# Optimization experiments

Hardware: AMD Instinct MI355X
Metric: run time of the kernel (lower is better)

Reference implementation:

```python
import jax, jax.numpy as jnp
import numpy as np

N_NODES = 50000
N_EDGES = 800000
N_GRAPHS = 512
D_NODE = 64
D_EDGE = 32
Z_DIM = 2 * D_NODE + D_EDGE  # 160


def setup_inputs() -> dict:
    key = jax.random.key(0)
    ks = jax.random.split(key, 12)
    inp = {
        'x': jax.random.normal(ks[0], (N_NODES, D_NODE), dtype=jnp.float32),
        'edge_index': jax.random.randint(ks[1], (2, N_EDGES), 0, N_NODES, dtype=jnp.int64),
        'edge_attr': jax.random.uniform(ks[2], (N_EDGES, D_EDGE), dtype=jnp.float32),
        'batch': jnp.sort(jax.random.randint(ks[3], (N_NODES,), 0, N_GRAPHS, dtype=jnp.int64)),
        'Wf1': jax.random.normal(ks[4], (Z_DIM, D_NODE), dtype=jnp.float32) * 0.05,
        'bf1': jnp.zeros((D_NODE,), dtype=jnp.float32),
        'Ws1': jax.random.normal(ks[5], (Z_DIM, D_NODE), dtype=jnp.float32) * 0.05,
        'bs1': jnp.zeros((D_NODE,), dtype=jnp.float32),
        'Wf2': jax.random.normal(ks[6], (Z_DIM, D_NODE), dtype=jnp.float32) * 0.05,
        'bf2': jnp.zeros((D_NODE,), dtype=jnp.float32),
        'Ws2': jax.random.normal(ks[7], (Z_DIM, D_NODE), dtype=jnp.float32) * 0.05,
        'bs2': jnp.zeros((D_NODE,), dtype=jnp.float32),
        'W_out': jax.random.normal(ks[8], (D_NODE, 1), dtype=jnp.float32) * 0.05,
        'b_out': jnp.zeros((1,), dtype=jnp.float32),
    }
    return inp


def _cgconv(x, edge_index, edge_attr, Wf, bf, Ws, bs):
    # PyG CGConv: out_i = x_i + sum_{j in N(i)} sigmoid(lin_f(z_ij)) * softplus(lin_s(z_ij))
    # with z_ij = [x_i, x_j, e_ij]; source_to_target flow: j=edge_index[0], i=edge_index[1]
    src, dst = edge_index[0], edge_index[1]
    z = jnp.concatenate([x[dst], x[src], edge_attr], axis=-1)  # [E, 2d+dim]
    msg = jax.nn.sigmoid(z @ Wf + bf) * jax.nn.softplus(z @ Ws + bs)  # [E, d]
    aggr = jax.ops.segment_sum(msg, dst, num_segments=x.shape[0])
    return x + aggr


def reference(x, edge_index, edge_attr, batch, Wf1, bf1, Ws1, bs1, Wf2, bf2, Ws2, bs2, W_out, b_out):
    h = _cgconv(x, edge_index, edge_attr, Wf1, bf1, Ws1, bs1)
    h = _cgconv(h, edge_index, edge_attr, Wf2, bf2, Ws2, bs2)
    pooled = jax.ops.segment_sum(h, batch, num_segments=N_GRAPHS)  # global_add_pool [G, d]
    out = pooled @ W_out + b_out  # [G, 1]
    return out
```

## Files before the change

### kernel.cpp

```cpp
#include <hip/hip_runtime.h>
#include <math.h>

#define N_NODES 50000
#define N_EDGES 800000
#define N_GRAPHS 512
#define D 64
#define DE 32
#define NB_SCAN 196
#define NSTR 136
#define NB_SCAT 3125
#define NB_FUSED 4689
#define NB_EDGE 1563


typedef __attribute__((ext_vector_type(8))) short short8;
typedef __attribute__((ext_vector_type(4))) float floatx4;
union Frag { short8 s; unsigned u[4]; };
union U4   { uint4 v; unsigned u[4]; };

__device__ inline unsigned pk_bf16(float lo, float hi) {
    unsigned a = __float_as_uint(lo);
    unsigned b = __float_as_uint(hi);
    a = (a + 0x7FFFu + ((a >> 16) & 1u)) >> 16;
    b = (b + 0x7FFFu + ((b >> 16) & 1u)) >> 16;
    return a | (b << 16);
}
__device__ inline unsigned short bf16_1(float v) {
    unsigned a = __float_as_uint(v);
    return (unsigned short)((a + 0x7FFFu + ((a >> 16) & 1u)) >> 16);
}
__device__ inline float upk(unsigned u16) { return __uint_as_float(u16 << 16); }

__global__ __launch_bounds__(256) void setup_kernel(
    const float* __restrict__ Wf1, const float* __restrict__ Ws1,
    const float* __restrict__ Wf2, const float* __restrict__ Ws2,
    uint4* __restrict__ WpkNT, uint4* __restrict__ WpkE,
    int* __restrict__ deg, float* __restrict__ pooled)
{
    const int b = blockIdx.x;
    if (b >= 206) {
        int i = (b - 206) * 256 + threadIdx.x;
        if (i < N_GRAPHS * D) pooled[i] = 0.0f;
        return;
    }
    if (b >= 10) {
        int i = (b - 10) * 256 + threadIdx.x;
        if (i < N_NODES) deg[i] = 0;
        return;
    }
    const int layer = b / 5;
    const float* Wf = layer ? Wf2 : Wf1;
    const float* Ws = layer ? Ws2 : Ws1;
    const int i = (b % 5) * 256 + threadIdx.x;
    if (i < 1024) {
        const int p    = i >> 9;
        const int cbi  = (i >> 6) & 7;
        const int l    = i & 63;
        const int n16  = l & 15, quad = l >> 4, kc = quad * 8;
        const int col  = cbi * 16 + n16;
        const int j    = col >> 1;
        const float* Wsel = (col & 1) ? Ws : Wf;
        const int rbase = p * 64;
        U4 b0, b1;
#pragma unroll
        for (int pp = 0; pp < 4; ++pp) {
            b0.u[pp] = pk_bf16(Wsel[(rbase + kc + 2 * pp) * 64 + j],
                               Wsel[(rbase + kc + 2 * pp + 1) * 64 + j]);
            b1.u[pp] = pk_bf16(Wsel[(rbase + 32 + kc + 2 * pp) * 64 + j],
                               Wsel[(rbase + 32 + kc + 2 * pp + 1) * 64 + j]);
        }
        uint4* o = WpkNT + ((size_t)layer * 1024 + i) * 2;
        o[0] = b0.v; o[1] = b1.v;
    } else if (i < 1280) {
        const int k  = i - 1024;
        const int jb = k >> 6;
        const int l  = k & 63;
        const int n16 = l & 15, quad = l >> 4, c0 = quad * 8;
        const int j = jb * 16 + n16;
        U4 bf_, bs_;
#pragma unroll
        for (int pp = 0; pp < 4; ++pp) {
            bf_.u[pp] = pk_bf16(Wf[(128 + c0 + 2 * pp) * 64 + j],
                                Wf[(128 + c0 + 2 * pp + 1) * 64 + j]);
            bs_.u[pp] = pk_bf16(Ws[(128 + c0 + 2 * pp) * 64 + j],
                                Ws[(128 + c0 + 2 * pp + 1) * 64 + j]);
        }
        uint4* o = WpkE + ((size_t)layer * 256 + k) * 2;
        o[0] = bf_.v; o[1] = bs_.v;
    }
}

__global__ __launch_bounds__(256) void hist_kernel(
    const int* __restrict__ ei, int* __restrict__ deg, int* __restrict__ rank)
{
    int e = blockIdx.x * 256 + threadIdx.x;
    rank[e] = atomicAdd(&deg[ei[N_EDGES + e]], 1);
}

__global__ __launch_bounds__(256) void scan1(
    const int* __restrict__ deg, int* __restrict__ off, int* __restrict__ tsum)
{
    __shared__ int s[256];
    int i = blockIdx.x * 256 + threadIdx.x;
    s[threadIdx.x] = (i < N_NODES) ? deg[i] : 0;
    __syncthreads();
    if (threadIdx.x == 0) {
        int run = 0;
        for (int k = 0; k < 256; ++k) { int t = s[k]; s[k] = run; run += t; }
        tsum[blockIdx.x] = run;
    }
    __syncthreads();
    if (i < N_NODES) off[i] = s[threadIdx.x];
}

__global__ __launch_bounds__(256) void scan23(
    int* __restrict__ off, const int* __restrict__ tsum)
{
    __shared__ int pfx;
    if (threadIdx.x == 0) {
        int run = 0;
        for (int k = 0; k < (int)blockIdx.x; ++k) run += tsum[k];
        pfx = run;
    }
    __syncthreads();
    int i = blockIdx.x * 256 + threadIdx.x;
    if (i < N_NODES) off[i] += pfx;
    if (i == N_NODES) off[i] = N_EDGES;
}

__global__ __launch_bounds__(256) void fused_scatter_nt(
    const int* __restrict__ ei, const int* __restrict__ off,
    const int* __restrict__ rank, const float* __restrict__ ea,
    unsigned short* __restrict__ eaS, int2* __restrict__ sd_sorted,
    const float* __restrict__ H,
    const float* __restrict__ bf, const float* __restrict__ bs,
    const uint4* __restrict__ Wpk,
    unsigned short* __restrict__ Tdst, unsigned short* __restrict__ Tsrc,
    float* __restrict__ hinit)
{
    __shared__ unsigned short lt[4][16 * NSTR];
    const int k = blockIdx.x;

    if ((k % 3) != 2) {
        const int sid = k - (k / 3);
        if (sid >= NB_SCAT) return;
        int e = sid * 256 + threadIdx.x;
        int s = ei[e];
        int d = ei[N_EDGES + e];
        int pos = off[d] + rank[e];
        sd_sorted[pos] = make_int2(s, d);

        const float4* src4 = (const float4*)(ea + (size_t)e * 32);
        uint4* dst16 = (uint4*)(eaS + (size_t)pos * 32);
#pragma unroll
        for (int q = 0; q < 2; ++q) {
            float4 v0 = src4[4 * q + 0];
            float4 v1 = src4[4 * q + 1];
            float4 v2 = src4[4 * q + 2];
            float4 v3 = src4[4 * q + 3];
            uint4 o0;
            o0.x = pk_bf16(v0.x, v0.y); o0.y = pk_bf16(v0.z, v0.w);
            o0.z = pk_bf16(v1.x, v1.y); o0.w = pk_bf16(v1.z, v1.w);
            uint4 o1;
            o1.x = pk_bf16(v2.x, v2.y); o1.y = pk_bf16(v2.z, v2.w);
            o1.z = pk_bf16(v3.x, v3.y); o1.w = pk_bf16(v3.z, v3.w);
            dst16[2 * q + 0] = o0;
            dst16[2 * q + 1] = o1;
        }
        return;
    }

    const int lane = threadIdx.x & 63;
    const int wid  = threadIdx.x >> 6;
    const int n16  = lane & 15;
    const int quad = lane >> 4;
    const int kc   = quad * 8;
    unsigned short* L = lt[wid];

    const int gid = (k / 3) * 4 + wid;
    const int NW  = (N_NODES / 16) * 2;
    if (gid >= NW) return;
    const int ntile = gid >> 1;
    const int part  = gid & 1;
    unsigned short* Tout = part ? Tsrc : Tdst;

    const float* hrow = H + (size_t)(ntile * 16 + n16) * D;
    float4 q0 = *(const float4*)(hrow + kc);
    float4 q1 = *(const float4*)(hrow + kc + 4);
    float4 q2 = *(const float4*)(hrow + 32 + kc);
    float4 q3 = *(const float4*)(hrow + 32 + kc + 4);
    Frag a0, a1;
    a0.u[0] = pk_bf16(q0.x, q0.y); a0.u[1] = pk_bf16(q0.z, q0.w);
    a0.u[2] = pk_bf16(q1.x, q1.y); a0.u[3] = pk_bf16(q1.z, q1.w);
    a1.u[0] = pk_bf16(q2.x, q2.y); a1.u[1] = pk_bf16(q2.z, q2.w);
    a1.u[2] = pk_bf16(q3.x, q3.y); a1.u[3] = pk_bf16(q3.z, q3.w);

    if (part == 0) {
        float4* hp = (float4*)(hinit + (size_t)(ntile * 16 + n16) * D);
        hp[quad * 2]     = q0;
        hp[quad * 2 + 1] = q1;
        hp[8 + quad * 2] = q2;
        hp[9 + quad * 2] = q3;
    }

#pragma unroll
    for (int cbi = 0; cbi < 8; ++cbi) {
        const int col   = cbi * 16 + n16;
        const int sflag = col & 1;
        const int j     = col >> 1;

        Frag b0, b1;
        {
            const uint4* bp = Wpk + ((size_t)(part * 512 + cbi * 64 + lane)) * 2;
            *(uint4*)&b0 = bp[0];
            *(uint4*)&b1 = bp[1];
        }
        float bias = 0.0f;
        if (part == 0) bias = sflag ? bs[j] : bf[j];

        floatx4 acc = {bias, bias, bias, bias};
        acc = __builtin_amdgcn_mfma_f32_16x16x32_bf16(a0.s, b0.s, acc, 0, 0, 0);
        acc = __builtin_amdgcn_mfma_f32_16x16x32_bf16(a1.s, b1.s, acc, 0, 0, 0);

#pragma unroll
        for (int r = 0; r < 4; ++r)
            L[(quad * 4 + r) * NSTR + col] = bf16_1(acc[r]);
    }

#pragma unroll
    for (int it = 0; it < 4; ++it) {
        const int node_l = it * 4 + quad;
        const int c8     = n16 * 8;
        uint4 v = *(const uint4*)(L + node_l * NSTR + c8);
        *(uint4*)(Tout + (size_t)(ntile * 16 + node_l) * 128 + c8) = v;
    }
}

__global__ __launch_bounds__(256) void node_transform_mfma(
    const float* __restrict__ H,
    const float* __restrict__ bf,
    const float* __restrict__ bs,
    const uint4* __restrict__ Wpk,
    unsigned short* __restrict__ Tdst,
    unsigned short* __restrict__ Tsrc,
    float* __restrict__ hinit)
{
    __shared__ unsigned short lt[4][16 * NSTR];
    const int lane = threadIdx.x & 63;
    const int wid  = threadIdx.x >> 6;
    const int n16  = lane & 15;
    const int quad = lane >> 4;
    const int kc   = quad * 8;
    unsigned short* L = lt[wid];

    const int gid = blockIdx.x * 4 + wid;
    const int NW  = (N_NODES / 16) * 2;
    if (gid >= NW) return;
    const int ntile = gid >> 1;
    const int part  = gid & 1;
    unsigned short* Tout = part ? Tsrc : Tdst;

    const float* hrow = H + (size_t)(ntile * 16 + n16) * D;
    float4 q0 = *(const float4*)(hrow + kc);
    float4 q1 = *(const float4*)(hrow + kc + 4);
    float4 q2 = *(const float4*)(hrow + 32 + kc);
    float4 q3 = *(const float4*)(hrow + 32 + kc + 4);
    Frag a0, a1;
    a0.u[0] = pk_bf16(q0.x, q0.y); a0.u[1] = pk_bf16(q0.z, q0.w);
    a0.u[2] = pk_bf16(q1.x, q1.y); a0.u[3] = pk_bf16(q1.z, q1.w);
    a1.u[0] = pk_bf16(q2.x, q2.y); a1.u[1] = pk_bf16(q2.z, q2.w);
    a1.u[2] = pk_bf16(q3.x, q3.y); a1.u[3] = pk_bf16(q3.z, q3.w);

    if (part == 0) {
        float4* hp = (float4*)(hinit + (size_t)(ntile * 16 + n16) * D);
        hp[quad * 2]     = q0;
        hp[quad * 2 + 1] = q1;
        hp[8 + quad * 2] = q2;
        hp[9 + quad * 2] = q3;
    }

#pragma unroll
    for (int cbi = 0; cbi < 8; ++cbi) {
        const int col   = cbi * 16 + n16;
        const int sflag = col & 1;
        const int j     = col >> 1;

        Frag b0, b1;
        {
            const uint4* bp = Wpk + ((size_t)(part * 512 + cbi * 64 + lane)) * 2;
            *(uint4*)&b0 = bp[0];
            *(uint4*)&b1 = bp[1];
        }
        float bias = 0.0f;
        if (part == 0) bias = sflag ? bs[j] : bf[j];

        floatx4 acc = {bias, bias, bias, bias};
        acc = __builtin_amdgcn_mfma_f32_16x16x32_bf16(a0.s, b0.s, acc, 0, 0, 0);
        acc = __builtin_amdgcn_mfma_f32_16x16x32_bf16(a1.s, b1.s, acc, 0, 0, 0);

#pragma unroll
        for (int r = 0; r < 4; ++r)
            L[(quad * 4 + r) * NSTR + col] = bf16_1(acc[r]);
    }

#pragma unroll
    for (int it = 0; it < 4; ++it) {
        const int node_l = it * 4 + quad;
        const int c8     = n16 * 8;
        uint4 v = *(const uint4*)(L + node_l * NSTR + c8);
        *(uint4*)(Tout + (size_t)(ntile * 16 + node_l) * 128 + c8) = v;
    }
}

__global__ __launch_bounds__(256) void edge_message_mfma(
    const unsigned short* __restrict__ Tdst,
    const unsigned short* __restrict__ Tsrc,
    const unsigned short* __restrict__ eaS,
    const int2* __restrict__ sd_sorted,
    const uint4* __restrict__ WpkE,
    float* __restrict__ hout)
{
    const int lane = threadIdx.x & 63;
    const int wid  = threadIdx.x >> 6;
    const int n16  = lane & 15;
    const int quad = lane >> 4;
    const int c0   = quad * 8;

    Frag bfr[4], bsr[4];
#pragma unroll
    for (int jb = 0; jb < 4; ++jb) {
        *(uint4*)&bfr[jb] = WpkE[((size_t)(jb * 64 + lane)) * 2 + 0];
        *(uint4*)&bsr[jb] = WpkE[((size_t)(jb * 64 + lane)) * 2 + 1];
    }

    const int nwg = gridDim.x;
    const int xcd = blockIdx.x & 7;
    const int idx = blockIdx.x >> 3;
    const int q   = nwg >> 3, rr = nwg & 7;
    const int sb  = (xcd < rr ? xcd * (q + 1) : rr * (q + 1) + (xcd - rr) * q) + idx;
    const int w   = sb * 4 + wid;
    if (w >= 6250) return;
    const int base0 = w * 128;

    const floatx4 zero = {0.0f, 0.0f, 0.0f, 0.0f};

    int cur_d = -1;
    float dfl0 = 0.f, dfl1 = 0.f, dfl2 = 0.f, dfl3 = 0.f;
    float dfh0 = 0.f, dfh1 = 0.f, dfh2 = 0.f, dfh3 = 0.f;
    float acc0 = 0.f, acc1 = 0.f, acc2 = 0.f, acc3 = 0.f;

#pragma unroll 1
    for (int g = 0; g < 2; ++g) {
        const int base = base0 + g * 64;

        const int4* sdp4 = (const int4*)(sd_sorted + base + quad * 16);
        int4 sdq[8];
#pragma unroll
        for (int i = 0; i < 8; ++i) sdq[i] = sdp4[i];

#define SV(e) ((((e) & 1) != 0) ? sdq[(e) >> 1].z : sdq[(e) >> 1].x)
#define DV(e) ((((e) & 1) != 0) ? sdq[(e) >> 1].w : sdq[(e) >> 1].y)

        const unsigned short* aptr =
            eaS + (size_t)(base + (n16 >> 2) * 16 + (n16 & 3)) * 32 + c0;
        Frag af;
        af.s = *(const short8*)aptr;

        unsigned sbuf[2][4][4];
#pragma unroll
        for (int r = 0; r < 4; ++r) {
            const unsigned* srow = (const unsigned*)(Tsrc + (size_t)SV(r) * 128);
            sbuf[0][r][0] = srow[n16];
            sbuf[0][r][1] = srow[16 + n16];
            sbuf[0][r][2] = srow[32 + n16];
            sbuf[0][r][3] = srow[48 + n16];
        }

#pragma unroll
        for (int tt = 0; tt < 4; ++tt) {
            const int cb = tt & 1, nb = cb ^ 1;
            if (tt < 3) {
#pragma unroll
                for (int r = 0; r < 4; ++r) {
                    const unsigned* srow =
                        (const unsigned*)(Tsrc + (size_t)SV(4 * (tt + 1) + r) * 128);
                    sbuf[nb][r][0] = srow[n16];
                    sbuf[nb][r][1] = srow[16 + n16];
                    sbuf[nb][r][2] = srow[32 + n16];
                    sbuf[nb][r][3] = srow[48 + n16];
                }
            }

            floatx4 accf[4], accs[4];
#pragma unroll
            for (int jb = 0; jb < 4; ++jb) {
                accf[jb] = __builtin_amdgcn_mfma_f32_16x16x32_bf16(af.s, bfr[jb].s, zero, 0, 0, 0);
                accs[jb] = __builtin_amdgcn_mfma_f32_16x16x32_bf16(af.s, bsr[jb].s, zero, 0, 0, 0);
            }
            if (tt < 3) af.s = *(const short8*)(aptr + (tt + 1) * 128);

#pragma unroll
            for (int r = 0; r < 4; ++r) {
                const int dv = DV(4 * tt + r);
                if (dv != cur_d) {
                    if (cur_d >= 0) {
                        float* hp = hout + (size_t)cur_d * D + n16;
                        atomicAdd(hp +  0, acc0);
                        atomicAdd(hp + 16, acc1);
                        atomicAdd(hp + 32, acc2);
                        atomicAdd(hp + 48, acc3);
                    }
                    cur_d = dv;
                    const unsigned* drow = (const unsigned*)(Tdst + (size_t)dv * 128);
                    unsigned t0 = drow[n16];
                    unsigned t1 = drow[16 + n16];
                    unsigned t2 = drow[32 + n16];
                    unsigned t3 = drow[48 + n16];
                    dfl0 = upk(t0 & 0xFFFFu); dfh0 = upk(t0 >> 16);
                    dfl1 = upk(t1 & 0xFFFFu); dfh1 = upk(t1 >> 16);
                    dfl2 = upk(t2 & 0xFFFFu); dfh2 = upk(t2 >> 16);
                    dfl3 = upk(t3 & 0xFFFFu); dfh3 = upk(t3 >> 16);
                    acc0 = acc1 = acc2 = acc3 = 0.f;
                }
#pragma unroll
                for (int jb = 0; jb < 4; ++jb) {
                    float dl = (jb == 0) ? dfl0 : (jb == 1) ? dfl1 : (jb == 2) ? dfl2 : dfl3;
                    float dh = (jb == 0) ? dfh0 : (jb == 1) ? dfh1 : (jb == 2) ? dfh2 : dfh3;
                    unsigned sv = sbuf[cb][r][jb];
                    float vf = accf[jb][r] + dl + upk(sv & 0xFFFFu);
                    float vs = accs[jb][r] + dh + upk(sv >> 16);
                    float sig = __builtin_amdgcn_rcpf(1.0f + __expf(-vf));
                    float spl = fmaxf(vs, 0.0f) + __logf(1.0f + __expf(-fabsf(vs)));
                    float msg = sig * spl;
                    if      (jb == 0) acc0 += msg;
                    else if (jb == 1) acc1 += msg;
                    else if (jb == 2) acc2 += msg;
                    else              acc3 += msg;
                }
            }
        }
#undef SV
#undef DV
    }
    {
        float* hp = hout + (size_t)cur_d * D + n16;
        atomicAdd(hp +  0, acc0);
        atomicAdd(hp + 16, acc1);
        atomicAdd(hp + 32, acc2);
        atomicAdd(hp + 48, acc3);
    }
}

__global__ __launch_bounds__(256) void pool_kernel(
    const float* __restrict__ h,
    const int* __restrict__ batch,
    float* __restrict__ pooled)
{
    const int lane = threadIdx.x & 63;
    const int wid  = threadIdx.x >> 6;
    const int w = blockIdx.x * 4 + wid;
    const int n0 = w * 16;
    if (n0 >= N_NODES) return;
    const int nend = (n0 + 16 < N_NODES) ? (n0 + 16) : N_NODES;

    int cur = batch[n0];
    float acc = 0.0f;
    for (int n = n0; n < nend; ++n) {
        int b = batch[n];
        float v = h[(size_t)n * D + lane];
        if (b != cur) {
            atomicAdd(&pooled[(size_t)cur * D + lane], acc);
            cur = b; acc = v;
        } else {
            acc += v;
        }
    }
    atomicAdd(&pooled[(size_t)cur * D + lane], acc);
}

__global__ __launch_bounds__(256) void out_kernel(
    const float* __restrict__ pooled,
    const float* __restrict__ Wout,
    const float* __restrict__ bout,
    float* __restrict__ out)
{
    const int g = blockIdx.x * blockDim.x + threadIdx.x;
    if (g >= N_GRAPHS) return;
    float acc = bout[0];
#pragma unroll
    for (int j = 0; j < D; ++j) acc = fmaf(pooled[(size_t)g * D + j], Wout[j], acc);
    out[g] = acc;
}

extern "C" void kernel_launch(void* const* d_in, const int* in_sizes, int n_in,
                              void* d_out, int out_size, void* d_ws, size_t ws_size,
                              hipStream_t stream) {
    const float* x     = (const float*)d_in[0];
    const int*   ei    = (const int*)  d_in[1];
    const float* ea    = (const float*)d_in[2];
    const int*   batch = (const int*)  d_in[3];
    const float* Wf1   = (const float*)d_in[4];
    const float* bf1   = (const float*)d_in[5];
    const float* Ws1   = (const float*)d_in[6];
    const float* bs1   = (const float*)d_in[7];
    const float* Wf2   = (const float*)d_in[8];
    const float* bf2   = (const float*)d_in[9];
    const float* Ws2   = (const float*)d_in[10];
    const float* bs2   = (const float*)d_in[11];
    const float* Wout  = (const float*)d_in[12];
    const float* bout  = (const float*)d_in[13];
    float* out = (float*)d_out;

    char* base = (char*)d_ws;
    size_t o = 0;
    unsigned short* Tdst = (unsigned short*)(base + o); o += (size_t)N_NODES * 128 * 2;
    unsigned short* Tsrc = (unsigned short*)(base + o); o += (size_t)N_NODES * 128 * 2;
    unsigned short* eaS  = (unsigned short*)(base + o); o += (size_t)N_EDGES * 32 * 2;
    float* h1     = (float*)(base + o); o += (size_t)N_NODES * D * 4;
    float* h2     = (float*)(base + o); o += (size_t)N_NODES * D * 4;
    float* pooled = (float*)(base + o); o += (size_t)N_GRAPHS * D * 4;
    int* deg  = (int*)(base + o); o += (size_t)N_NODES * 4;
    int* off  = (int*)(base + o); o += (size_t)(N_NODES + 1) * 4;
    int* tsum = (int*)(base + o); o += 256 * 4;
    int2* sd_sorted = (int2*)(base + o); o += (size_t)N_EDGES * 8;
    int* rank = (int*)(base + o); o += (size_t)N_EDGES * 4;
    uint4* WpkNT = (uint4*)(base + o); o += (size_t)2 * 1024 * 2 * 16;
    uint4* WpkE  = (uint4*)(base + o); o += (size_t)2 * 256 * 2 * 16;

    setup_kernel<<<334, 256, 0, stream>>>(Wf1, Ws1, Wf2, Ws2,
                                          WpkNT, WpkE, deg, pooled);
    hist_kernel<<<NB_SCAT, 256, 0, stream>>>(ei, deg, rank);
    scan1<<<NB_SCAN, 256, 0, stream>>>(deg, off, tsum);
    scan23<<<NB_SCAN, 256, 0, stream>>>(off, tsum);
    fused_scatter_nt<<<NB_FUSED, 256, 0, stream>>>(
        ei, off, rank, ea, eaS, sd_sorted,
        x, bf1, bs1, WpkNT, Tdst, Tsrc, h1);
    edge_message_mfma<<<NB_EDGE, 256, 0, stream>>>(Tdst, Tsrc, eaS, sd_sorted,
                                                   WpkE, h1);
    node_transform_mfma<<<1563, 256, 0, stream>>>(h1, bf2, bs2, WpkNT + 2048,
                                                  Tdst, Tsrc, h2);
    edge_message_mfma<<<NB_EDGE, 256, 0, stream>>>(Tdst, Tsrc, eaS, sd_sorted,
                                                   WpkE + 512, h2);
    pool_kernel<<<782, 256, 0, stream>>>(h2, batch, pooled);
    out_kernel<<<2, 256, 0, stream>>>(pooled, Wout, bout, out);
}
```

Before: 449.0 us.

## Privatize degree histogram into 8 sub-counters and halve per-wave edge chunk

The degree histogram is split into 8 per-block-group copies to reduce atomic contention on popular destination nodes. The scan merges the copies and emits per-sub offsets, so the CSR order stays deterministic. Separately, each edge-message wave now handles 64 edges instead of 128, doubling the grid to 3125 blocks for more parallelism, at the cost of more boundary atomics and repeated weight-fragment loads. The change also adds memory traffic for zeroing and scanning eight copies of the histogram.

```diff
diff --git a/kernel.cpp b/kernel.cpp
--- a/kernel.cpp
+++ b/kernel.cpp
@@ -10,7 +10,6 @@
 #define NSTR 136
 #define NB_SCAT 3125
 #define NB_FUSED 4689
-#define NB_EDGE 1563
 
 
 typedef __attribute__((ext_vector_type(8))) short short8;
@@ -35,17 +34,17 @@
     const float* __restrict__ Wf1, const float* __restrict__ Ws1,
     const float* __restrict__ Wf2, const float* __restrict__ Ws2,
     uint4* __restrict__ WpkNT, uint4* __restrict__ WpkE,
-    int* __restrict__ deg, float* __restrict__ pooled)
+    int* __restrict__ deg8, float* __restrict__ pooled)
 {
     const int b = blockIdx.x;
-    if (b >= 206) {
-        int i = (b - 206) * 256 + threadIdx.x;
+    if (b >= 1573) {
+        int i = (b - 1573) * 256 + threadIdx.x;
         if (i < N_GRAPHS * D) pooled[i] = 0.0f;
         return;
     }
     if (b >= 10) {
         int i = (b - 10) * 256 + threadIdx.x;
-        if (i < N_NODES) deg[i] = 0;
+        if (i < 8 * N_NODES) deg8[i] = 0;
         return;
     }
     const int layer = b / 5;
@@ -91,18 +90,24 @@
 }
 
 __global__ __launch_bounds__(256) void hist_kernel(
-    const int* __restrict__ ei, int* __restrict__ deg, int* __restrict__ rank)
-{
+    const int* __restrict__ ei, int* __restrict__ deg8, int* __restrict__ r8)
+{
+    const int sub = blockIdx.x & 7;
     int e = blockIdx.x * 256 + threadIdx.x;
-    rank[e] = atomicAdd(&deg[ei[N_EDGES + e]], 1);
+    r8[e] = atomicAdd(&deg8[sub * N_NODES + ei[N_EDGES + e]], 1);
 }
 
 __global__ __launch_bounds__(256) void scan1(
-    const int* __restrict__ deg, int* __restrict__ off, int* __restrict__ tsum)
+    const int* __restrict__ deg8, int* __restrict__ off, int* __restrict__ tsum)
 {
     __shared__ int s[256];
     int i = blockIdx.x * 256 + threadIdx.x;
-    s[threadIdx.x] = (i < N_NODES) ? deg[i] : 0;
+    int tot = 0;
+    if (i < N_NODES) {
+#pragma unroll
+        for (int ss = 0; ss < 8; ++ss) tot += deg8[ss * N_NODES + i];
+    }
+    s[threadIdx.x] = tot;
     __syncthreads();
     if (threadIdx.x == 0) {
         int run = 0;
@@ -114,7 +119,8 @@
 }
 
 __global__ __launch_bounds__(256) void scan23(
-    int* __restrict__ off, const int* __restrict__ tsum)
+    const int* __restrict__ off, const int* __restrict__ tsum,
+    const int* __restrict__ deg8, int* __restrict__ off8)
 {
     __shared__ int pfx;
     if (threadIdx.x == 0) {
@@ -124,13 +130,19 @@
     }
     __syncthreads();
     int i = blockIdx.x * 256 + threadIdx.x;
-    if (i < N_NODES) off[i] += pfx;
-    if (i == N_NODES) off[i] = N_EDGES;
+    if (i < N_NODES) {
+        int running = off[i] + pfx;
+#pragma unroll
+        for (int ss = 0; ss < 8; ++ss) {
+            off8[ss * N_NODES + i] = running;
+            running += deg8[ss * N_NODES + i];
+        }
+    }
 }
 
 __global__ __launch_bounds__(256) void fused_scatter_nt(
-    const int* __restrict__ ei, const int* __restrict__ off,
-    const int* __restrict__ rank, const float* __restrict__ ea,
+    const int* __restrict__ ei, const int* __restrict__ off8,
+    const int* __restrict__ r8, const float* __restrict__ ea,
     unsigned short* __restrict__ eaS, int2* __restrict__ sd_sorted,
     const float* __restrict__ H,
     const float* __restrict__ bf, const float* __restrict__ bs,
@@ -144,10 +156,11 @@
     if ((k % 3) != 2) {
         const int sid = k - (k / 3);
         if (sid >= NB_SCAT) return;
+        const int sub = sid & 7;
         int e = sid * 256 + threadIdx.x;
         int s = ei[e];
         int d = ei[N_EDGES + e];
-        int pos = off[d] + rank[e];
+        int pos = off8[sub * N_NODES + d] + r8[e];
         sd_sorted[pos] = make_int2(s, d);
 
         const float4* src4 = (const float4*)(ea + (size_t)e * 32);
@@ -339,109 +352,103 @@
     const int q   = nwg >> 3, rr = nwg & 7;
     const int sb  = (xcd < rr ? xcd * (q + 1) : rr * (q + 1) + (xcd - rr) * q) + idx;
     const int w   = sb * 4 + wid;
-    if (w >= 6250) return;
-    const int base0 = w * 128;
+    const int base = w * 64;
 
     const floatx4 zero = {0.0f, 0.0f, 0.0f, 0.0f};
+
+    const int4* sdp4 = (const int4*)(sd_sorted + base + quad * 16);
+    int4 sdq[8];
+#pragma unroll
+    for (int i = 0; i < 8; ++i) sdq[i] = sdp4[i];
+
+#define SV(e) ((((e) & 1) != 0) ? sdq[(e) >> 1].z : sdq[(e) >> 1].x)
+#define DV(e) ((((e) & 1) != 0) ? sdq[(e) >> 1].w : sdq[(e) >> 1].y)
+
+    const unsigned short* aptr =
+        eaS + (size_t)(base + (n16 >> 2) * 16 + (n16 & 3)) * 32 + c0;
+    Frag af;
+    af.s = *(const short8*)aptr;
+
+    unsigned sbuf[2][4][4];
+#pragma unroll
+    for (int r = 0; r < 4; ++r) {
+        const unsigned* srow = (const unsigned*)(Tsrc + (size_t)SV(r) * 128);
+        sbuf[0][r][0] = srow[n16];
+        sbuf[0][r][1] = srow[16 + n16];
+        sbuf[0][r][2] = srow[32 + n16];
+        sbuf[0][r][3] = srow[48 + n16];
+    }
 
     int cur_d = -1;
     float dfl0 = 0.f, dfl1 = 0.f, dfl2 = 0.f, dfl3 = 0.f;
     float dfh0 = 0.f, dfh1 = 0.f, dfh2 = 0.f, dfh3 = 0.f;
     float acc0 = 0.f, acc1 = 0.f, acc2 = 0.f, acc3 = 0.f;
 
-#pragma unroll 1
-    for (int g = 0; g < 2; ++g) {
-        const int base = base0 + g * 64;
-
-        const int4* sdp4 = (const int4*)(sd_sorted + base + quad * 16);
-        int4 sdq[8];
-#pragma unroll
-        for (int i = 0; i < 8; ++i) sdq[i] = sdp4[i];
-
-#define SV(e) ((((e) & 1) != 0) ? sdq[(e) >> 1].z : sdq[(e) >> 1].x)
-#define DV(e) ((((e) & 1) != 0) ? sdq[(e) >> 1].w : sdq[(e) >> 1].y)
-
-        const unsigned short* aptr =
-            eaS + (size_t)(base + (n16 >> 2) * 16 + (n16 & 3)) * 32 + c0;
-        Frag af;
-        af.s = *(const short8*)aptr;
-
-        unsigned sbuf[2][4][4];
+#pragma unroll
+    for (int tt = 0; tt < 4; ++tt) {
+        const int cb = tt & 1, nb = cb ^ 1;
+        if (tt < 3) {
+#pragma unroll
+            for (int r = 0; r < 4; ++r) {
+                const unsigned* srow =
+                    (const unsigned*)(Tsrc + (size_t)SV(4 * (tt + 1) + r) * 128);
+                sbuf[nb][r][0] = srow[n16];
+                sbuf[nb][r][1] = srow[16 + n16];
+                sbuf[nb][r][2] = srow[32 + n16];
+                sbuf[nb][r][3] = srow[48 + n16];
+            }
+        }
+
+        floatx4 accf[4], accs[4];
+#pragma unroll
+        for (int jb = 0; jb < 4; ++jb) {
+            accf[jb] = __builtin_amdgcn_mfma_f32_16x16x32_bf16(af.s, bfr[jb].s, zero, 0, 0, 0);
+            accs[jb] = __builtin_amdgcn_mfma_f32_16x16x32_bf16(af.s, bsr[jb].s, zero, 0, 0, 0);
+        }
+        if (tt < 3) af.s = *(const short8*)(aptr + (tt + 1) * 128);
+
 #pragma unroll
         for (int r = 0; r < 4; ++r) {
-            const unsigned* srow = (const unsigned*)(Tsrc + (size_t)SV(r) * 128);
-            sbuf[0][r][0] = srow[n16];
-            sbuf[0][r][1] = srow[16 + n16];
-            sbuf[0][r][2] = srow[32 + n16];
-            sbuf[0][r][3] = srow[48 + n16];
-        }
-
-#pragma unroll
-        for (int tt = 0; tt < 4; ++tt) {
-            const int cb = tt & 1, nb = cb ^ 1;
-            if (tt < 3) {
-#pragma unroll
-                for (int r = 0; r < 4; ++r) {
-                    const unsigned* srow =
-                        (const unsigned*)(Tsrc + (size_t)SV(4 * (tt + 1) + r) * 128);
-                    sbuf[nb][r][0] = srow[n16];
-                    sbuf[nb][r][1] = srow[16 + n16];
-                    sbuf[nb][r][2] = srow[32 + n16];
-                    sbuf[nb][r][3] = srow[48 + n16];
+            const int dv = DV(4 * tt + r);
+            if (dv != cur_d) {
+                if (cur_d >= 0) {
+                    float* hp = hout + (size_t)cur_d * D + n16;
+                    atomicAdd(hp +  0, acc0);
+                    atomicAdd(hp + 16, acc1);
+                    atomicAdd(hp + 32, acc2);
+                    atomicAdd(hp + 48, acc3);
                 }
+                cur_d = dv;
+                const unsigned* drow = (const unsigned*)(Tdst + (size_t)dv * 128);
+                unsigned t0 = drow[n16];
+                unsigned t1 = drow[16 + n16];
+                unsigned t2 = drow[32 + n16];
+                unsigned t3 = drow[48 + n16];
+                dfl0 = upk(t0 & 0xFFFFu); dfh0 = upk(t0 >> 16);
+                dfl1 = upk(t1 & 0xFFFFu); dfh1 = upk(t1 >> 16);
+                dfl2 = upk(t2 & 0xFFFFu); dfh2 = upk(t2 >> 16);
+                dfl3 = upk(t3 & 0xFFFFu); dfh3 = upk(t3 >> 16);
+                acc0 = acc1 = acc2 = acc3 = 0.f;
             }
-
-            floatx4 accf[4], accs[4];
 #pragma unroll
             for (int jb = 0; jb < 4; ++jb) {
-                accf[jb] = __builtin_amdgcn_mfma_f32_16x16x32_bf16(af.s, bfr[jb].s, zero, 0, 0, 0);
-                accs[jb] = __builtin_amdgcn_mfma_f32_16x16x32_bf16(af.s, bsr[jb].s, zero, 0, 0, 0);
+                float dl = (jb == 0) ? dfl0 : (jb == 1) ? dfl1 : (jb == 2) ? dfl2 : dfl3;
+                float dh = (jb == 0) ? dfh0 : (jb == 1) ? dfh1 : (jb == 2) ? dfh2 : dfh3;
+                unsigned sv = sbuf[cb][r][jb];
+                float vf = accf[jb][r] + dl + upk(sv & 0xFFFFu);
+                float vs = accs[jb][r] + dh + upk(sv >> 16);
+                float sig = __builtin_amdgcn_rcpf(1.0f + __expf(-vf));
+                float spl = fmaxf(vs, 0.0f) + __logf(1.0f + __expf(-fabsf(vs)));
+                float msg = sig * spl;
+                if      (jb == 0) acc0 += msg;
+                else if (jb == 1) acc1 += msg;
+                else if (jb == 2) acc2 += msg;
+                else              acc3 += msg;
             }
-            if (tt < 3) af.s = *(const short8*)(aptr + (tt + 1) * 128);
-
-#pragma unroll
-            for (int r = 0; r < 4; ++r) {
-                const int dv = DV(4 * tt + r);
-                if (dv != cur_d) {
-                    if (cur_d >= 0) {
-                        float* hp = hout + (size_t)cur_d * D + n16;
-                        atomicAdd(hp +  0, acc0);
-                        atomicAdd(hp + 16, acc1);
-                        atomicAdd(hp + 32, acc2);
-                        atomicAdd(hp + 48, acc3);
-                    }
-                    cur_d = dv;
-                    const unsigned* drow = (const unsigned*)(Tdst + (size_t)dv * 128);
-                    unsigned t0 = drow[n16];
-                    unsigned t1 = drow[16 + n16];
-                    unsigned t2 = drow[32 + n16];
-                    unsigned t3 = drow[48 + n16];
-                    dfl0 = upk(t0 & 0xFFFFu); dfh0 = upk(t0 >> 16);
-                    dfl1 = upk(t1 & 0xFFFFu); dfh1 = upk(t1 >> 16);
-                    dfl2 = upk(t2 & 0xFFFFu); dfh2 = upk(t2 >> 16);
-                    dfl3 = upk(t3 & 0xFFFFu); dfh3 = upk(t3 >> 16);
-                    acc0 = acc1 = acc2 = acc3 = 0.f;
-                }
-#pragma unroll
-                for (int jb = 0; jb < 4; ++jb) {
-                    float dl = (jb == 0) ? dfl0 : (jb == 1) ? dfl1 : (jb == 2) ? dfl2 : dfl3;
-                    float dh = (jb == 0) ? dfh0 : (jb == 1) ? dfh1 : (jb == 2) ? dfh2 : dfh3;
-                    unsigned sv = sbuf[cb][r][jb];
-                    float vf = accf[jb][r] + dl + upk(sv & 0xFFFFu);
-                    float vs = accs[jb][r] + dh + upk(sv >> 16);
-                    float sig = __builtin_amdgcn_rcpf(1.0f + __expf(-vf));
-                    float spl = fmaxf(vs, 0.0f) + __logf(1.0f + __expf(-fabsf(vs)));
-                    float msg = sig * spl;
-                    if      (jb == 0) acc0 += msg;
-                    else if (jb == 1) acc1 += msg;
-                    else if (jb == 2) acc2 += msg;
-                    else              acc3 += msg;
-                }
-            }
-        }
+        }
+    }
 #undef SV
 #undef DV
-    }
     {
         float* hp = hout + (size_t)cur_d * D + n16;
         atomicAdd(hp +  0, acc0);
@@ -519,27 +526,28 @@
     float* h1     = (float*)(base + o); o += (size_t)N_NODES * D * 4;
     float* h2     = (float*)(base + o); o += (size_t)N_NODES * D * 4;
     float* pooled = (float*)(base + o); o += (size_t)N_GRAPHS * D * 4;
-    int* deg  = (int*)(base + o); o += (size_t)N_NODES * 4;
+    int* deg8 = (int*)(base + o); o += (size_t)8 * N_NODES * 4;
     int* off  = (int*)(base + o); o += (size_t)(N_NODES + 1) * 4;
+    int* off8 = (int*)(base + o); o += (size_t)8 * N_NODES * 4;
     int* tsum = (int*)(base + o); o += 256 * 4;
     int2* sd_sorted = (int2*)(base + o); o += (size_t)N_EDGES * 8;
-    int* rank = (int*)(base + o); o += (size_t)N_EDGES * 4;
+    int* r8 = (int*)(base + o); o += (size_t)N_EDGES * 4;
     uint4* WpkNT = (uint4*)(base + o); o += (size_t)2 * 1024 * 2 * 16;
     uint4* WpkE  = (uint4*)(base + o); o += (size_t)2 * 256 * 2 * 16;
 
-    setup_kernel<<<334, 256, 0, stream>>>(Wf1, Ws1, Wf2, Ws2,
-                                          WpkNT, WpkE, deg, pooled);
-    hist_kernel<<<NB_SCAT, 256, 0, stream>>>(ei, deg, rank);
-    scan1<<<NB_SCAN, 256, 0, stream>>>(deg, off, tsum);
-    scan23<<<NB_SCAN, 256, 0, stream>>>(off, tsum);
+    setup_kernel<<<1701, 256, 0, stream>>>(Wf1, Ws1, Wf2, Ws2,
+                                           WpkNT, WpkE, deg8, pooled);
+    hist_kernel<<<NB_SCAT, 256, 0, stream>>>(ei, deg8, r8);
+    scan1<<<NB_SCAN, 256, 0, stream>>>(deg8, off, tsum);
+    scan23<<<NB_SCAN, 256, 0, stream>>>(off, tsum, deg8, off8);
     fused_scatter_nt<<<NB_FUSED, 256, 0, stream>>>(
-        ei, off, rank, ea, eaS, sd_sorted,
+        ei, off8, r8, ea, eaS, sd_sorted,
         x, bf1, bs1, WpkNT, Tdst, Tsrc, h1);
-    edge_message_mfma<<<NB_EDGE, 256, 0, stream>>>(Tdst, Tsrc, eaS, sd_sorted,
+    edge_message_mfma<<<NB_SCAT, 256, 0, stream>>>(Tdst, Tsrc, eaS, sd_sorted,
                                                    WpkE, h1);
     node_transform_mfma<<<1563, 256, 0, stream>>>(h1, bf2, bs2, WpkNT + 2048,
                                                   Tdst, Tsrc, h2);
-    edge_message_mfma<<<NB_EDGE, 256, 0, stream>>>(Tdst, Tsrc, eaS, sd_sorted,
+    edge_message_mfma<<<NB_SCAT, 256, 0, stream>>>(Tdst, Tsrc, eaS, sd_sorted,
                                                    WpkE + 512, h2);
     pool_kernel<<<782, 256, 0, stream>>>(h2, batch, pooled);
     out_kernel<<<2, 256, 0, stream>>>(pooled, Wout, bout, out);
```

Result: faster. 439.9 us (-2.0%).
